# Kernel optimization log

Hardware: AMD Instinct MI355X
Metric: run time of the kernel (lower is better)

## Reference

```python
import jax, jax.numpy as jnp
import numpy as np

B, D_IN = 8192, 4096
H1, H2, LAT = 2048, 1024, 256
NQ, NL = 16, 2


def setup_inputs() -> dict:
    key = jax.random.key(0)
    ks = jax.random.split(key, 16)
    def lin(k, fan_in, fan_out):
        k1, k2 = jax.random.split(k)
        s = 1.0 / np.sqrt(fan_in)
        W = jax.random.uniform(k1, (fan_out, fan_in), jnp.float32, -s, s)
        b = jax.random.uniform(k2, (fan_out,), jnp.float32, -s, s)
        return W, b
    x = jax.random.normal(ks[0], (B, D_IN), jnp.float32)
    We1, be1 = lin(ks[1], D_IN, H1)
    We2, be2 = lin(ks[2], H1, H2)
    We3, be3 = lin(ks[3], H2, LAT)
    P = jax.random.normal(ks[4], (NL, NQ, 3), jnp.float32)  # ansatz params (rx,ry,rz)
    Wd1, bd1 = lin(ks[5], NQ, H2)
    Wd2, bd2 = lin(ks[6], H2, H1)
    Wd3, bd3 = lin(ks[7], H1, D_IN)
    return {"x": x, "We1": We1, "be1": be1, "We2": We2, "be2": be2,
            "We3": We3, "be3": be3, "P": P, "Wd1": Wd1, "bd1": bd1,
            "Wd2": Wd2, "bd2": bd2, "Wd3": Wd3, "bd3": bd3}


def _quantum_block(latent, P):
    """Exact simulation of the per-qubit circuit (all gates single-qubit, so the
    2^n statevector factorizes into per-qubit 2-vectors (a,b) over |0>,|1>).
    latent: (B, LAT), P: (NL, NQ, 3). Returns Z-expectations (B, NQ)."""
    nq = P.shape[1]
    th = latent[:, :nq]  # encoding RY angles, (B, NQ)
    # RY(th)|0> = cos(th/2)|0> + sin(th/2)|1>
    a = jnp.cos(th / 2).astype(jnp.complex64)  # (B, NQ)
    b = jnp.sin(th / 2).astype(jnp.complex64)
    for l in range(P.shape[0]):
        # RX
        t = P[l, :, 0] / 2
        c, s = jnp.cos(t).astype(jnp.complex64), jnp.sin(t).astype(jnp.complex64)
        a, b = c * a - 1j * s * b, -1j * s * a + c * b
        # RY
        t = P[l, :, 1] / 2
        c, s = jnp.cos(t).astype(jnp.complex64), jnp.sin(t).astype(jnp.complex64)
        a, b = c * a - s * b, s * a + c * b
        # RZ
        t = P[l, :, 2] / 2
        ph = jnp.exp(-1j * t.astype(jnp.complex64))
        a, b = a * ph, b * jnp.conj(ph)
    z = (a.real ** 2 + a.imag ** 2) - (b.real ** 2 + b.imag ** 2)
    return z.astype(latent.dtype)


def reference(x, We1, be1, We2, be2, We3, be3, P,
              Wd1, bd1, Wd2, bd2, Wd3, bd3):
    h = jax.nn.relu(x @ We1.T + be1)
    h = jax.nn.relu(h @ We2.T + be2)
    latent = h @ We3.T + be3            # (B, LAT)
    refined = _quantum_block(latent, P)  # (B, NQ)
    h = jax.nn.relu(refined @ Wd1.T + bd1)
    h = jax.nn.relu(h @ Wd2.T + bd2)
    return h @ Wd3.T + bd3              # (B, D_IN)
```

## Files before the change

kernel.cpp:

```cpp
#include <hip/hip_runtime.h>

typedef __attribute__((ext_vector_type(8))) short bf16x8;
typedef __attribute__((ext_vector_type(4))) float f32x4;

__device__ __forceinline__ unsigned short f2bf(float f) {
    union { float f; unsigned int u; } v; v.f = f;
    unsigned int u = v.u;
    unsigned int r = (u + 0x7FFFu + ((u >> 16) & 1u)) >> 16;
    return (unsigned short)r;
}
__device__ __forceinline__ float bf2f(unsigned short b) {
    union { unsigned int u; float f; } v; v.u = ((unsigned int)b) << 16;
    return v.f;
}

#define GL16(g, l)                                                             \
    __builtin_amdgcn_global_load_lds(                                          \
        (__attribute__((address_space(1))) void*)(void*)(g),                   \
        (__attribute__((address_space(3))) void*)(void*)(l), 16, 0, 0)

#define BAR()  __builtin_amdgcn_s_barrier()
#define LGKM0() asm volatile("s_waitcnt lgkmcnt(0)" ::: "memory")

struct Cast5 {
    const float *s0, *s1, *s2, *s3, *s4;
    unsigned short *d0, *d1, *d2, *d3, *d4;
    int n0, n1, n2, n3, total;
};
__global__ void castall(Cast5 a) {
    int stride = gridDim.x * blockDim.x;
    for (int i = blockIdx.x * blockDim.x + threadIdx.x; i < a.total; i += stride) {
        int j = i; const float* s; unsigned short* d;
        if (j < a.n0) { s = a.s0; d = a.d0; }
        else { j -= a.n0;
            if (j < a.n1) { s = a.s1; d = a.d1; }
            else { j -= a.n1;
                if (j < a.n2) { s = a.s2; d = a.d2; }
                else { j -= a.n2;
                    if (j < a.n3) { s = a.s3; d = a.d3; }
                    else { j -= a.n3; s = a.s4; d = a.d4; } } } }
        float4 v = ((const float4*)s)[j];
        ushort4 o;
        o.x = f2bf(v.x); o.y = f2bf(v.y); o.z = f2bf(v.z); o.w = f2bf(v.w);
        ((ushort4*)d)[j] = o;
    }
}


template<int RELU, int OUT_BF16, int MP>
__global__ __launch_bounds__(512, 2) void gemm8p(
    const unsigned short* __restrict__ A,
    const unsigned short* __restrict__ Bm,
    const float* __restrict__ bias,
    void* __restrict__ Cout,
    int N, int K, int NT)
{
    constexpr int AHU  = MP * 2048;
    constexpr int BOFF = MP * 8192;
    __shared__ __align__(16) unsigned short lds[MP * 8192 + 32768];

    const int tid  = threadIdx.x;
    const int lane = tid & 63;
    const int w    = tid >> 6;
    const int wm   = w >> 2;
    const int wn   = w & 3;
    const int bm   = blockIdx.y;
    const int bn   = blockIdx.x;

    const unsigned short* gA = A  + (long)bm * (MP * 64) * K;
    const unsigned short* gB = Bm + (long)bn * 256 * K;

    const int sr0 = tid >> 3;
    const int so0 = (((tid & 7) * 16) ^ ((sr0 & 7) << 4)) >> 1;
    const int loff = (sr0 * K + so0) * 2;
    const int ch1  = K * 128;
    const int lb0 = (w * 64) * 8;
    const int lb1 = (512 + w * 64) * 8;

    const int cl  = lane & 15;
    const int g16 = (lane >> 4) * 16;
    const int sw  = (cl & 7) << 4;
    const int cK0 = (g16 ^ sw) >> 1;
    const int cK1 = ((64 + g16) ^ sw) >> 1;
    const int arb = wm * (MP * 16) + cl;
    const int brb = wn * 32 + cl;
    const int aIdx0 = (arb * 64 + cK0) * 2;
    const int aIdx1 = (arb * 64 + cK1) * 2;
    const int bIdx0 = (BOFF + brb * 64 + cK0) * 2;
    const int bIdx1 = (BOFF + brb * 64 + cK1) * 2;

    f32x4  acc[2][2][MP][2] = {};
    bf16x8 a0[MP][2], a1[MP][2], b0[2][2], b1[2][2];

#define GLA_(SP, DI) do {                                                      \
        GL16((const char*)(SP) + loff, &lds[0] + (DI) + lb0);                  \
        if constexpr (MP == 4) {                                               \
            GL16((const char*)(SP) + loff + ch1, &lds[0] + (DI) + lb1); }      \
    } while (0)
#define GLB_(SP, DI) do {                                                      \
        GL16((const char*)(SP) + loff, &lds[0] + (DI) + lb0);                  \
        GL16((const char*)(SP) + loff + ch1, &lds[0] + (DI) + lb1);            \
    } while (0)

#define READA_(AR, MH, PAR) do {                                               \
        _Pragma("unroll") for (int mp_ = 0; mp_ < MP; ++mp_) {                 \
            AR[mp_][0] = *(const bf16x8*)((const char*)lds + aIdx0 +           \
                         (((PAR)*2+(MH))*AHU*2 + mp_*2048));                   \
            AR[mp_][1] = *(const bf16x8*)((const char*)lds + aIdx1 +           \
                         (((PAR)*2+(MH))*AHU*2 + mp_*2048));                   \
        } } while (0)
#define READB_(BR, NH, PAR) do {                                               \
        _Pragma("unroll") for (int np_ = 0; np_ < 2; ++np_) {                  \
            BR[np_][0] = *(const bf16x8*)((const char*)lds + bIdx0 +           \
                         (((PAR)*2+(NH))*16384 + np_*2048));                   \
            BR[np_][1] = *(const bf16x8*)((const char*)lds + bIdx1 +           \
                         (((PAR)*2+(NH))*16384 + np_*2048));                   \
        } } while (0)
#define QUAD(mh, nh, AR, BR) do {                                              \
        __builtin_amdgcn_s_setprio(1);                                         \
        _Pragma("unroll") for (int kk_ = 0; kk_ < 2; ++kk_)                    \
        _Pragma("unroll") for (int mp_ = 0; mp_ < MP; ++mp_)                   \
        _Pragma("unroll") for (int np_ = 0; np_ < 2; ++np_)                    \
            acc[mh][nh][mp_][np_] = __builtin_amdgcn_mfma_f32_16x16x32_bf16(   \
                AR[mp_][kk_], BR[np_][kk_], acc[mh][nh][mp_][np_], 0, 0, 0);   \
        __builtin_amdgcn_s_setprio(0);                                         \
    } while (0)
#define VMW() do {                                                             \
        if constexpr (MP == 4) asm volatile("s_waitcnt vmcnt(6)" ::: "memory");\
        else                   asm volatile("s_waitcnt vmcnt(5)" ::: "memory");\
    } while (0)

    GLB_(gB,                      BOFF + 0);
    GLA_(gA,                      0);
    GLB_(gB + (long)128 * K,      BOFF + 8192);
    GLA_(gA + (long)(MP*32) * K,  AHU);
    GLB_(gB + 64,                 BOFF + 2*8192);
    GLA_(gA + 64,                 2*AHU);
    GLB_(gB + (long)128 * K + 64, BOFF + 3*8192);
    VMW();
    BAR();
    READA_(a0, 0, 0);
    READB_(b0, 0, 0);

    const unsigned short* sA1 = gA + (long)(MP*32) * K + 64;
    const unsigned short* sA0 = gA + 128;
    const unsigned short* sB0 = gB + 128;
    const unsigned short* sB1 = gB + (long)128 * K + 128;

#define KTILE(T, PAR) do {                                                     \
        const int adv1_ = ((T) + 2 < NT) ? 64 : 0;                             \
        const int adv2_ = ((T) + 3 < NT) ? 64 : 0;                             \
                                                                       \
        READA_(a1, 1, PAR);                                                    \
        GLA_(sA1, (((PAR)^1)*2+1)*AHU); sA1 += adv1_;                          \
        BAR();                                                                 \
        QUAD(0, 0, a0, b0);                                                    \
                                                                       \
        READB_(b1, 1, PAR);                                                    \
        GLB_(sB0, BOFF + (PAR)*2*8192); sB0 += adv2_;                          \
        VMW();                                                                 \
        BAR();                                                                 \
        QUAD(0, 1, a0, b1);                                                    \
                                                                       \
        READA_(a0, 0, (PAR)^1);                                                \
        GLA_(sA0, (PAR)*2*AHU); sA0 += adv2_;                                  \
        BAR();                                                                 \
        QUAD(1, 1, a1, b1);                                                    \
                                                                       \
        GLB_(sB1, BOFF + ((PAR)*2+1)*8192); sB1 += adv2_;                      \
        VMW();                                                                 \
        BAR();                                                                 \
        QUAD(1, 0, a1, b0);                                                    \
        READB_(b0, 0, (PAR)^1);                                                \
    } while (0)

    for (int t = 0; t < NT; t += 2) {
        KTILE(t, 0);
        KTILE(t + 1, 1);
    }

    asm volatile("s_waitcnt vmcnt(0)" ::: "memory");
    BAR();

    const int r4 = (lane >> 4) * 4;
    float bv[2][2];
    #pragma unroll
    for (int nh = 0; nh < 2; ++nh)
        #pragma unroll
        for (int np = 0; np < 2; ++np)
            bv[nh][np] = bias[(long)bn * 256 + nh * 128 + wn * 32 + np * 16 + cl];

    if (OUT_BF16) {
        unsigned short* epi = lds;
        #pragma unroll
        for (int h = 0; h < 2; ++h) {
            if (h) { LGKM0(); BAR(); }
            #pragma unroll
            for (int mp = 0; mp < MP; ++mp)
                #pragma unroll
                for (int nh = 0; nh < 2; ++nh)
                    #pragma unroll
                    for (int np = 0; np < 2; ++np)
                        #pragma unroll
                        for (int r = 0; r < 4; ++r) {
                            float v = acc[h][nh][mp][np][r] + bv[nh][np];
                            if (RELU) v = fmaxf(v, 0.f);
                            int lrow = wm * (MP * 16) + mp * 16 + r4 + r;
                            int lcol = nh * 128 + wn * 32 + np * 16 + cl;
                            epi[lrow * 264 + lcol] = f2bf(v);
                        }
            LGKM0();
            BAR();
            long rowg0 = (long)bm * (MP * 64) + h * (MP * 32);
            #pragma unroll
            for (int i = 0; i < 2 * MP; ++i) {
                int row = (tid >> 5) + i * 16;
                int cc  = (tid & 31) * 8;
                bf16x8 v8 = *(const bf16x8*)&epi[row * 264 + cc];
                *(bf16x8*)((unsigned short*)Cout + (rowg0 + row) * (long)N + (long)bn * 256 + cc) = v8;
            }
        }
    } else {
        #pragma unroll
        for (int mh = 0; mh < 2; ++mh)
            #pragma unroll
            for (int mp = 0; mp < MP; ++mp) {
                long grow = (long)bm * (MP * 64) + mh * (MP * 32) + wm * (MP * 16) + mp * 16 + r4;
                #pragma unroll
                for (int nh = 0; nh < 2; ++nh)
                    #pragma unroll
                    for (int np = 0; np < 2; ++np) {
                        long gcol = (long)bn * 256 + nh * 128 + wn * 32 + np * 16 + cl;
                        #pragma unroll
                        for (int r = 0; r < 4; ++r) {
                            float v = acc[mh][nh][mp][np][r] + bv[nh][np];
                            if (RELU) v = fmaxf(v, 0.f);
                            ((float*)Cout)[(grow + r) * (long)N + gcol] = v;
                        }
                    }
            }
    }
#undef GLA_
#undef GLB_
#undef READA_
#undef READB_
#undef QUAD
#undef VMW
#undef KTILE
}

__global__ __launch_bounds__(256) void latq_d1(
    const unsigned short* __restrict__ h2,
    const float* __restrict__ We3,
    const float* __restrict__ be3,
    const float* __restrict__ P,
    const float* __restrict__ Wd1,
    const float* __restrict__ bd1,
    unsigned short* __restrict__ h3)
{
    __shared__ float zsh[4][16];
    const int lane = threadIdx.x & 63;
    const int wv   = threadIdx.x >> 6;
    const long row = (long)blockIdx.x * 4 + wv;

    float hreg[16];
    const unsigned short* hr = h2 + row * 1024;
    #pragma unroll
    for (int j = 0; j < 16; ++j) hreg[j] = bf2f(hr[lane + 64 * j]);

    float myth = 0.f;
    #pragma unroll
    for (int q = 0; q < 16; ++q) {
        const float* wq = We3 + q * 1024;
        float p = 0.f;
        #pragma unroll
        for (int j = 0; j < 16; ++j) p += hreg[j] * wq[lane + 64 * j];
        #pragma unroll
        for (int o = 32; o; o >>= 1) p += __shfl_xor(p, o, 64);
        if (lane == q) myth = p + be3[q];
    }

    if (lane < 16) {
        const int q = lane;
        float ar = cosf(0.5f * myth), ai = 0.f;
        float br = sinf(0.5f * myth), bi = 0.f;
        #pragma unroll
        for (int l = 0; l < 2; ++l) {
            const float* pp = P + (l * 16 + q) * 3;
            float t, c, s, ar2, ai2, br2, bi2;
            t = 0.5f * pp[0]; c = cosf(t); s = sinf(t);
            ar2 = c * ar + s * bi;  ai2 = c * ai - s * br;
            br2 = c * br + s * ai;  bi2 = c * bi - s * ar;
            ar = ar2; ai = ai2; br = br2; bi = bi2;
            t = 0.5f * pp[1]; c = cosf(t); s = sinf(t);
            ar2 = c * ar - s * br;  ai2 = c * ai - s * bi;
            br2 = s * ar + c * br;  bi2 = s * ai + c * bi;
            ar = ar2; ai = ai2; br = br2; bi = bi2;
            t = 0.5f * pp[2]; c = cosf(t); s = sinf(t);
            ar2 = ar * c + ai * s;  ai2 = ai * c - ar * s;
            br2 = br * c - bi * s;  bi2 = bi * c + br * s;
            ar = ar2; ai = ai2; br = br2; bi = bi2;
        }
        zsh[wv][q] = ar * ar + ai * ai - (br * br + bi * bi);
    }
    __syncthreads();

    float z[16];
    #pragma unroll
    for (int q = 0; q < 16; ++q) z[q] = zsh[wv][q];

    unsigned short* orow = h3 + row * 1024;
    #pragma unroll
    for (int i = 0; i < 16; ++i) {
        int j = lane + 64 * i;
        const float4* wrow = (const float4*)(Wd1 + j * 16);
        float acc = bd1[j];
        #pragma unroll
        for (int qq = 0; qq < 4; ++qq) {
            float4 w4 = wrow[qq];
            acc += z[qq * 4 + 0] * w4.x + z[qq * 4 + 1] * w4.y
                 + z[qq * 4 + 2] * w4.z + z[qq * 4 + 3] * w4.w;
        }
        orow[j] = f2bf(fmaxf(acc, 0.f));
    }
}

extern "C" void kernel_launch(void* const* d_in, const int* in_sizes, int n_in,
                              void* d_out, int out_size, void* d_ws, size_t ws_size,
                              hipStream_t stream) {
    const float* x   = (const float*)d_in[0];
    const float* We1 = (const float*)d_in[1];
    const float* be1 = (const float*)d_in[2];
    const float* We2 = (const float*)d_in[3];
    const float* be2 = (const float*)d_in[4];
    const float* We3 = (const float*)d_in[5];
    const float* be3 = (const float*)d_in[6];
    const float* P   = (const float*)d_in[7];
    const float* Wd1 = (const float*)d_in[8];
    const float* bd1 = (const float*)d_in[9];
    const float* Wd2 = (const float*)d_in[10];
    const float* bd2 = (const float*)d_in[11];
    const float* Wd3 = (const float*)d_in[12];
    const float* bd3 = (const float*)d_in[13];

    const int B = 8192, DIN = 4096, NH1 = 2048, NH2 = 1024;

    char* w = (char*)d_ws;
    unsigned short* x_bf   = (unsigned short*)(w);
    unsigned short* h4     = x_bf;
    unsigned short* We1_bf = (unsigned short*)(w + 67108864L);
    unsigned short* We2_bf = (unsigned short*)(w + 83886080L);
    unsigned short* Wd2_bf = (unsigned short*)(w + 88080384L);
    unsigned short* Wd3_bf = (unsigned short*)(w + 92274688L);
    unsigned short* h1     = (unsigned short*)(w + 109051904L);
    unsigned short* h3     = h1;
    unsigned short* h2     = (unsigned short*)(w + 142606336L);

    Cast5 ca;
    ca.s0 = x;   ca.d0 = x_bf;   ca.n0 = (int)((long)B * DIN / 4);
    ca.s1 = We1; ca.d1 = We1_bf; ca.n1 = (int)((long)NH1 * DIN / 4);
    ca.s2 = We2; ca.d2 = We2_bf; ca.n2 = (int)((long)NH2 * NH1 / 4);
    ca.s3 = Wd2; ca.d3 = Wd2_bf; ca.n3 = (int)((long)NH1 * NH2 / 4);
    ca.s4 = Wd3; ca.d4 = Wd3_bf;
    ca.total = ca.n0 + ca.n1 + ca.n2 + ca.n3 + (int)((long)DIN * NH1 / 4);
    castall<<<2048, 256, 0, stream>>>(ca);

    gemm8p<1, 1, 4><<<dim3(NH1 / 256, B / 256), 512, 0, stream>>>(x_bf, We1_bf, be1, h1, NH1, DIN, DIN >> 6);
    gemm8p<1, 1, 2><<<dim3(NH2 / 256, B / 128), 512, 0, stream>>>(h1, We2_bf, be2, h2, NH2, NH1, NH1 >> 6);
    latq_d1<<<dim3(B / 4), 256, 0, stream>>>(h2, We3, be3, P, Wd1, bd1, h3);
    gemm8p<1, 1, 4><<<dim3(NH1 / 256, B / 256), 512, 0, stream>>>(h3, Wd2_bf, bd2, h4, NH1, NH2, NH2 >> 6);
    gemm8p<0, 0, 4><<<dim3(DIN / 256, B / 256), 512, 0, stream>>>(h4, Wd3_bf, bd3, d_out, DIN, NH1, NH1 >> 6);
}
```

Measured before the change: 387.9 us.

## Restructure GEMM K-loop pipeline with full-tile prefetch and explicit LDS waits

Reworks the double-buffered GEMM main loop. The prologue now prefetches both A halves for the first two K-tiles, and each K-tile reads its LDS fragments at the start of the tile instead of carrying them over from the previous one. Explicit lgkmcnt waits and extra barriers are placed around each MFMA quadrant, and the global-to-LDS issue points and vmcnt thresholds are adjusted to match. The aim is a simpler, race-free schedule with deeper global prefetch, at the cost of more barriers per tile and less overlap between LDS reads and MFMAs.

```diff
diff --git a/kernel.cpp b/kernel.cpp
--- a/kernel.cpp
+++ b/kernel.cpp
@@ -19,7 +19,7 @@
         (__attribute__((address_space(1))) void*)(void*)(g),                   \
         (__attribute__((address_space(3))) void*)(void*)(l), 16, 0, 0)
 
-#define BAR()  __builtin_amdgcn_s_barrier()
+#define BAR()   __builtin_amdgcn_s_barrier()
 #define LGKM0() asm volatile("s_waitcnt lgkmcnt(0)" ::: "memory")
 
 struct Cast5 {
@@ -125,53 +125,58 @@
                 AR[mp_][kk_], BR[np_][kk_], acc[mh][nh][mp_][np_], 0, 0, 0);   \
         __builtin_amdgcn_s_setprio(0);                                         \
     } while (0)
-#define VMW() do {                                                             \
-        if constexpr (MP == 4) asm volatile("s_waitcnt vmcnt(6)" ::: "memory");\
-        else                   asm volatile("s_waitcnt vmcnt(5)" ::: "memory");\
-    } while (0)
-
-    GLB_(gB,                      BOFF + 0);
-    GLA_(gA,                      0);
-    GLB_(gB + (long)128 * K,      BOFF + 8192);
-    GLA_(gA + (long)(MP*32) * K,  AHU);
-    GLB_(gB + 64,                 BOFF + 2*8192);
-    GLA_(gA + 64,                 2*AHU);
-    GLB_(gB + (long)128 * K + 64, BOFF + 3*8192);
-    VMW();
+#define VMT() do {                                                             \
+        if constexpr (MP == 4) asm volatile("s_waitcnt vmcnt(8)" ::: "memory");\
+        else                   asm volatile("s_waitcnt vmcnt(6)" ::: "memory");\
+    } while (0)
+
+    GLB_(gB,                          BOFF + 0);
+    GLA_(gA,                          0);
+    GLB_(gB + (long)128 * K,          BOFF + 8192);
+    GLA_(gA + (long)(MP*32) * K,      AHU);
+    GLB_(gB + 64,                     BOFF + 2*8192);
+    GLA_(gA + 64,                     2*AHU);
+    GLB_(gB + (long)128 * K + 64,     BOFF + 3*8192);
+    GLA_(gA + (long)(MP*32) * K + 64, 3*AHU);
+    VMT();
     BAR();
-    READA_(a0, 0, 0);
-    READB_(b0, 0, 0);
-
-    const unsigned short* sA1 = gA + (long)(MP*32) * K + 64;
+
     const unsigned short* sA0 = gA + 128;
+    const unsigned short* sA1 = gA + (long)(MP*32) * K + 128;
     const unsigned short* sB0 = gB + 128;
     const unsigned short* sB1 = gB + (long)128 * K + 128;
 
 #define KTILE(T, PAR) do {                                                     \
-        const int adv1_ = ((T) + 2 < NT) ? 64 : 0;                             \
-        const int adv2_ = ((T) + 3 < NT) ? 64 : 0;                             \
+        const int adv_ = ((T) + 3 < NT) ? 64 : 0;                              \
+                                                                       \
+        READA_(a0, 0, PAR);                                                    \
+        READB_(b0, 0, PAR);                                                    \
+        if constexpr (MP == 4) asm volatile("s_waitcnt lgkmcnt(8)" ::: "memory"); \
+        BAR();                                                                 \
+        LGKM0();                                                               \
+        QUAD(0, 0, a0, b0);                                                    \
+        BAR();                                                                 \
+                                                                       \
+        READB_(b1, 1, PAR);                                                    \
+        GLA_(sA0, (PAR)*2*AHU); sA0 += adv_;                                   \
+        BAR();                                                                 \
+        LGKM0();                                                               \
+        QUAD(0, 1, a0, b1);                                                    \
+        BAR();                                                                 \
                                                                        \
         READA_(a1, 1, PAR);                                                    \
-        GLA_(sA1, (((PAR)^1)*2+1)*AHU); sA1 += adv1_;                          \
-        BAR();                                                                 \
-        QUAD(0, 0, a0, b0);                                                    \
+        GLB_(sB0, BOFF + (PAR)*2*8192); sB0 += adv_;                           \
+        BAR();                                                                 \
+        LGKM0();                                                               \
+        QUAD(1, 1, a1, b1);                                                    \
+        BAR();                                                                 \
                                                                        \
-        READB_(b1, 1, PAR);                                                    \
-        GLB_(sB0, BOFF + (PAR)*2*8192); sB0 += adv2_;                          \
-        VMW();                                                                 \
-        BAR();                                                                 \
-        QUAD(0, 1, a0, b1);                                                    \
-                                                                       \
-        READA_(a0, 0, (PAR)^1);                                                \
-        GLA_(sA0, (PAR)*2*AHU); sA0 += adv2_;                                  \
-        BAR();                                                                 \
-        QUAD(1, 1, a1, b1);                                                    \
-                                                                       \
-        GLB_(sB1, BOFF + ((PAR)*2+1)*8192); sB1 += adv2_;                      \
-        VMW();                                                                 \
+        GLA_(sA1, ((PAR)*2+1)*AHU); sA1 += adv_;                               \
+        GLB_(sB1, BOFF + ((PAR)*2+1)*8192); sB1 += adv_;                       \
+        VMT();                                                                 \
         BAR();                                                                 \
         QUAD(1, 0, a1, b0);                                                    \
-        READB_(b0, 0, (PAR)^1);                                                \
+        BAR();                                                                 \
     } while (0)
 
     for (int t = 0; t < NT; t += 2) {
@@ -245,7 +250,7 @@
 #undef READA_
 #undef READB_
 #undef QUAD
-#undef VMW
+#undef VMT
 #undef KTILE
 }
 
```

Measured after the change: 415.0 us. 7.0% more time.
